# Optimization experiments

Measured on AMD Instinct MI355X. Metric: run time of the kernel, lower is better.

The kernel has to match this reference:

```python
import jax, jax.numpy as jnp
import numpy as np

N_NODES = 50000
N_EDGES = 800000
F_IN = 64
HID = 256
N_GRAPHS = 128
N_OUT = 24


def _sage_conv(x, src, dst, deg_inv, wl, bl, wr):
    # PyG SAGEConv (aggr='mean'): out = lin_l(mean_{j in N(i)} x_j) + lin_r(x_i)
    agg = jax.ops.segment_sum(x[src], dst, num_segments=x.shape[0]) * deg_inv
    return agg @ wl.T + bl + x @ wr.T


def setup_inputs() -> dict:
    key = jax.random.key(0)
    ks = jax.random.split(key, 16)
    x = jax.random.normal(ks[0], (N_NODES, F_IN), dtype=jnp.float32)
    edge_index = jax.random.randint(ks[1], (2, N_EDGES), 0, N_NODES, dtype=jnp.int64)
    batch = jnp.sort(jax.random.randint(ks[2], (N_NODES,), 0, N_GRAPHS, dtype=jnp.int64))

    def lin(k, fan_out, fan_in):
        bound = 1.0 / np.sqrt(fan_in)
        return jax.random.uniform(k, (fan_out, fan_in), jnp.float32, -bound, bound)

    inp = {
        'x': x, 'edge_index': edge_index, 'batch': batch,
        'w1l': lin(ks[3], HID, F_IN), 'b1': jnp.zeros((HID,), jnp.float32), 'w1r': lin(ks[4], HID, F_IN),
        'w2l': lin(ks[5], HID, HID), 'b2': jnp.zeros((HID,), jnp.float32), 'w2r': lin(ks[6], HID, HID),
        'w3l': lin(ks[7], HID, HID), 'b3': jnp.zeros((HID,), jnp.float32), 'w3r': lin(ks[8], HID, HID),
        'lin1_w': lin(ks[9], HID // 2, HID), 'lin1_b': jnp.zeros((HID // 2,), jnp.float32),
        'lin2_w': lin(ks[10], N_OUT, HID // 2), 'lin2_b': jnp.zeros((N_OUT,), jnp.float32),
    }
    return inp


def reference(x, edge_index, batch, w1l, b1, w1r, w2l, b2, w2r, w3l, b3, w3r,
              lin1_w, lin1_b, lin2_w, lin2_b):
    src, dst = edge_index[0], edge_index[1]
    deg = jax.ops.segment_sum(jnp.ones((src.shape[0],), jnp.float32), dst, num_segments=x.shape[0])
    deg_inv = (1.0 / jnp.maximum(deg, 1.0))[:, None]  # [N,1]

    h = jax.nn.relu(_sage_conv(x, src, dst, deg_inv, w1l, b1, w1r))
    h = jax.nn.relu(_sage_conv(h, src, dst, deg_inv, w2l, b2, w2r))
    h = jax.nn.relu(_sage_conv(h, src, dst, deg_inv, w3l, b3, w3r))

    # global mean pool over graphs
    pooled_sum = jax.ops.segment_sum(h, batch, num_segments=N_GRAPHS)
    counts = jax.ops.segment_sum(jnp.ones((h.shape[0],), jnp.float32), batch, num_segments=N_GRAPHS)
    pooled = pooled_sum / jnp.maximum(counts, 1.0)[:, None]

    g = jax.nn.relu(pooled @ lin1_w.T + lin1_b)
    return g @ lin2_w.T + lin2_b
```

## Files before the change

### kernel.cpp

```cpp
#include <hip/hip_runtime.h>

#define N_NODES 50000
#define M_PAD   50048
#define N_EDGES 800000
#define F_IN 64
#define HID 256
#define N_GRAPHS 128
#define N_OUT 24

typedef unsigned short ushort_t;
typedef __attribute__((ext_vector_type(8))) unsigned short us8;
typedef __attribute__((ext_vector_type(8))) __bf16 bf16x8;
typedef __attribute__((ext_vector_type(4))) float f32x4;

#define SLICE_US ((size_t)M_PAD * 32)

__device__ __forceinline__ unsigned short f2bf(float f) {
  unsigned u = __builtin_bit_cast(unsigned, f);
  return (unsigned short)((u + 0x7fffu + ((u >> 16) & 1u)) >> 16);
}
__device__ __forceinline__ float bf2f(unsigned short h) {
  return __builtin_bit_cast(float, (unsigned)h << 16);
}

__device__ __forceinline__ f32x4 mfma_bf16(us8 a, us8 b, f32x4 c) {
  return __builtin_amdgcn_mfma_f32_16x16x32_bf16(
      __builtin_bit_cast(bf16x8, a), __builtin_bit_cast(bf16x8, b), c, 0, 0, 0);
}

__device__ __forceinline__ void gload16(const ushort_t* g, ushort_t* l) {
  __builtin_amdgcn_global_load_lds(
      (const __attribute__((address_space(1))) void*)g,
      (__attribute__((address_space(3))) void*)l, 16, 0, 0);
}


__global__ void k_hist(const int* __restrict__ dst, int* __restrict__ deg_priv,
                       int* __restrict__ rank) {
  int e = blockIdx.x * 256 + threadIdx.x;
  if (e < N_EDGES) {
    int c = blockIdx.x & 7;
    rank[e] = atomicAdd(&deg_priv[c * N_NODES + dst[e]], 1);
  }
}

__global__ void k_gofs(const int* __restrict__ batch, int* __restrict__ gofs) {
  int t = threadIdx.x;
  if (t > N_GRAPHS) return;
  int lo = 0, hi = N_NODES;
  while (lo < hi) {
    int mid = (lo + hi) >> 1;
    if (batch[mid] < t) lo = mid + 1;
    else hi = mid;
  }
  gofs[t] = lo;
}

__global__ __launch_bounds__(1024) void k_scan1(int* __restrict__ deg_priv,
                                                int* __restrict__ deg,
                                                int* __restrict__ rowptr,
                                                int* __restrict__ partial) {
  __shared__ int s[1024];
  int t = threadIdx.x;
  int idx = blockIdx.x * 1024 + t;
  int v = 0;
  if (idx < N_NODES) {
    int run = 0;
#pragma unroll
    for (int c = 0; c < 8; ++c) {
      int dv = deg_priv[c * N_NODES + idx];
      deg_priv[c * N_NODES + idx] = run;
      run += dv;
    }
    deg[idx] = run;
    v = run;
  }
  s[t] = v;
  __syncthreads();
  for (int off = 1; off < 1024; off <<= 1) {
    int a = (t >= off) ? s[t - off] : 0;
    __syncthreads();
    s[t] += a;
    __syncthreads();
  }
  if (idx < N_NODES) rowptr[idx] = s[t] - v;
  if (t == 1023) partial[blockIdx.x] = s[1023];
}

__global__ void k_scan2(int* __restrict__ partial, int* __restrict__ rowptr) {
  __shared__ int s[64];
  int t = threadIdx.x;
  const int NB = (N_NODES + 1023) / 1024;
  int v = (t < NB) ? partial[t] : 0;
  s[t] = v;
  __syncthreads();
  for (int off = 1; off < 64; off <<= 1) {
    int a = (t >= off) ? s[t - off] : 0;
    __syncthreads();
    s[t] += a;
    __syncthreads();
  }
  if (t < NB) partial[t] = s[t] - v;
  if (t == NB - 1) rowptr[N_NODES] = s[t];
}

__global__ __launch_bounds__(1024) void k_scan3(const int* __restrict__ deg,
                                                const int* __restrict__ partial,
                                                int* __restrict__ rowptr,
                                                float* __restrict__ deg_inv) {
  int idx = blockIdx.x * 1024 + threadIdx.x;
  if (idx < N_NODES) {
    rowptr[idx] += partial[blockIdx.x];
    deg_inv[idx] = 1.0f / fmaxf((float)deg[idx], 1.0f);
  }
}

__global__ void k_place(const int* __restrict__ src, const int* __restrict__ dst,
                        const int* __restrict__ rowptr, const int* __restrict__ deg_priv,
                        const int* __restrict__ rank, int* __restrict__ esrc) {
  int e = blockIdx.x * 256 + threadIdx.x;
  if (e < N_EDGES) {
    int c = blockIdx.x & 7;
    int d = dst[e];
    esrc[rowptr[d] + deg_priv[c * N_NODES + d] + rank[e]] = src[e];
  }
}


__global__ void k_prep_x(const float* __restrict__ x, ushort_t* __restrict__ xio) {
  int g = blockIdx.x * 256 + threadIdx.x;
  if (g >= N_NODES * 8) return;
  int row = g >> 3, kb = g & 7;
  const float* p = x + (size_t)row * F_IN + kb * 8;
  us8 H, L;
#pragma unroll
  for (int i = 0; i < 8; ++i) {
    float f = p[i];
    unsigned short hi = f2bf(f);
    H[i] = hi;
    L[i] = f2bf(f - bf2f(hi));
  }
  size_t ob = (size_t)row * 128 + (size_t)((kb ^ (row & 7)) << 3);
  *(us8*)&xio[ob] = H;
  *(us8*)&xio[ob + 64] = L;
}

__global__ void k_prep_w(const float* __restrict__ w1lp, const float* __restrict__ w1rp,
                         const float* __restrict__ w2lp, const float* __restrict__ w2rp,
                         const float* __restrict__ w3lp, const float* __restrict__ w3rp,
                         ushort_t* __restrict__ wf1, ushort_t* __restrict__ wf2,
                         ushort_t* __restrict__ wf3) {
  int layer = blockIdx.z, side = blockIdx.y;
  const int Kg = (layer == 0) ? 8 : 32;
  const int qcs = Kg >> 2;
  int g = blockIdx.x * 256 + threadIdx.x;
  if (g >= 256 * Kg) return;
  const float* src = (layer == 0) ? (side ? w1rp : w1lp)
                   : (layer == 1) ? (side ? w2rp : w2lp)
                                  : (side ? w3rp : w3lp);
  ushort_t* dstf = (layer == 0) ? wf1 : (layer == 1) ? wf2 : wf3;
  int row = g / Kg, gb = g % Kg;
  const float* p = src + (size_t)row * (Kg * 8) + gb * 8;
  us8 H, L;
#pragma unroll
  for (int i = 0; i < 8; ++i) {
    float f = p[i];
    unsigned short hi = f2bf(f);
    H[i] = hi;
    L[i] = f2bf(f - bf2f(hi));
  }
  int nb2 = side * 16 + (row >> 4);
  int lane = (row & 15) + ((gb & 3) << 4);
  size_t base = ((size_t)(nb2 * qcs + (gb >> 2)) * 2) * 512 + lane * 8;
  *(us8*)&dstf[base] = H;
  *(us8*)&dstf[base + 512] = L;
}


__global__ __launch_bounds__(256) void k_agg64s(const float* __restrict__ x,
                                                const int* __restrict__ rowptr,
                                                const int* __restrict__ esrc,
                                                const float* __restrict__ deg_inv,
                                                ushort_t* __restrict__ oio) {
  int node = blockIdx.x * 4 + (threadIdx.x >> 6);
  if (node >= N_NODES) return;
  int lane = threadIdx.x & 63;
  int e0 = rowptr[node], e1 = rowptr[node + 1];
  float acc = 0.f;
  int e = e0;
  for (; e + 4 <= e1; e += 4) {
    int s0 = esrc[e], s1 = esrc[e + 1], s2 = esrc[e + 2], s3 = esrc[e + 3];
    float v0 = x[(size_t)s0 * F_IN + lane];
    float v1 = x[(size_t)s1 * F_IN + lane];
    float v2 = x[(size_t)s2 * F_IN + lane];
    float v3 = x[(size_t)s3 * F_IN + lane];
    acc += v0 + v1 + v2 + v3;
  }
  for (; e < e1; ++e) acc += x[(size_t)esrc[e] * F_IN + lane];
  acc *= deg_inv[node];
  unsigned short hi = f2bf(acc);
  unsigned short lo = f2bf(acc - bf2f(hi));
  size_t rb = (size_t)node * 128;
  int slot = ((lane >> 3) ^ (node & 7)) << 3;
  oio[rb + slot + (lane & 7)] = hi;
  oio[rb + 64 + slot + (lane & 7)] = lo;
}

__global__ __launch_bounds__(256) void k_agg256s(const ushort_t* __restrict__ hio,
                                                 const int* __restrict__ rowptr,
                                                 const int* __restrict__ esrc,
                                                 const float* __restrict__ deg_inv,
                                                 ushort_t* __restrict__ oio) {
  int c = blockIdx.x & 7;
  const ushort_t* hs = hio + (size_t)c * SLICE_US;
  ushort_t* os = oio + (size_t)c * SLICE_US;
  int q = threadIdx.x & 3;
  int ns = threadIdx.x >> 2;
  for (int base = (blockIdx.x >> 3) * 64; base < N_NODES; base += 16384) {
    int node = base + ns;
    if (node >= N_NODES) continue;
    int e0 = rowptr[node], e1 = rowptr[node + 1];
    float a[8] = {0.f, 0.f, 0.f, 0.f, 0.f, 0.f, 0.f, 0.f};
    int e = e0;
#pragma unroll 1
    for (; e + 4 <= e1; e += 4) {
      int s0 = esrc[e], s1 = esrc[e + 1], s2 = esrc[e + 2], s3 = esrc[e + 3];
      us8 v0 = *(const us8*)&hs[(size_t)s0 * 32 + ((q ^ (s0 & 3)) << 3)];
      us8 v1 = *(const us8*)&hs[(size_t)s1 * 32 + ((q ^ (s1 & 3)) << 3)];
      us8 v2 = *(const us8*)&hs[(size_t)s2 * 32 + ((q ^ (s2 & 3)) << 3)];
      us8 v3 = *(const us8*)&hs[(size_t)s3 * 32 + ((q ^ (s3 & 3)) << 3)];
#pragma unroll
      for (int i = 0; i < 8; ++i)
        a[i] += (bf2f(v0[i]) + bf2f(v1[i])) + (bf2f(v2[i]) + bf2f(v3[i]));
    }
    for (; e < e1; ++e) {
      int s = esrc[e];
      us8 v = *(const us8*)&hs[(size_t)s * 32 + ((q ^ (s & 3)) << 3)];
#pragma unroll
      for (int i = 0; i < 8; ++i) a[i] += bf2f(v[i]);
    }
    float di = deg_inv[node];
    us8 H;
#pragma unroll
    for (int i = 0; i < 8; ++i) H[i] = f2bf(a[i] * di);
    __builtin_nontemporal_store(
        H, (us8*)&os[(size_t)node * 32 + ((q ^ (node & 3)) << 3)]);
  }
}


template <int SA>
__global__ __launch_bounds__(256, 2) void k_gemm_mfma(
    const ushort_t* __restrict__ A1, int k1g, const ushort_t* __restrict__ w1f,
    const ushort_t* __restrict__ A2, int k2g, const ushort_t* __restrict__ w2f,
    const float* __restrict__ bias, ushort_t* __restrict__ oio,
    float* __restrict__ ofp, int mode) {
  __shared__ __align__(16) ushort_t ldsA[2][SA ? 16384 : 8192];

  int t = threadIdx.x;
  int wv = t >> 6, lane = t & 63;
  int fr = lane & 15, kq = lane >> 4;
  int bm = blockIdx.x;
  int rowA0 = bm * 128;

  f32x4 acc[8][4];
#pragma unroll
  for (int m = 0; m < 8; ++m)
#pragma unroll
    for (int n = 0; n < 4; ++n) acc[m][n] = (f32x4)0.f;

  const int ns1 = k1g >> 3, ns2 = k2g >> 3, ns = ns1 + ns2;
  const int lj = lane & 7, lr8 = lane >> 3;

  auto stage = [&](int buf, int s) {
    bool p2 = s >= ns1;
    const ushort_t* A = p2 ? A2 : A1;
    int Kg = p2 ? k2g : k1g;
    int sl = p2 ? (s - ns1) : s;
#pragma unroll
    for (int i = 0; i < 4; ++i) {
      int row = wv * 32 + i * 8 + lr8;
      int R = rowA0 + row;
      int lo = (wv * 32 + i * 8) * 64;
      if (SA) {
        size_t offA = ((size_t)R * (Kg * 2) + sl * 8 + lj) * 8;
        gload16(A + offA, &ldsA[buf][lo]);
        gload16(A + offA + (size_t)Kg * 8, &ldsA[buf][8192 + lo]);
      } else {
        size_t offA = (size_t)(sl * 2 + ((lj >> 2) ^ ((R >> 2) & 1))) * SLICE_US +
                      (size_t)R * 32 + (size_t)((lj & 3) << 3);
        gload16(A + offA, &ldsA[buf][lo]);
      }
    }
  };

  stage(0, 0);
  __syncthreads();
  int cur = 0;

  for (int s = 0; s < ns; ++s) {
    bool p2 = s >= ns1;
    const ushort_t* Wf = p2 ? w2f : w1f;
    int sl = p2 ? (s - ns1) : s;
    int qcs = (p2 ? k2g : k1g) >> 2;

    us8 bh[2][4], bl[2][4];
#pragma unroll
    for (int kc = 0; kc < 2; ++kc)
#pragma unroll
      for (int n = 0; n < 4; ++n) {
        size_t base = ((size_t)((wv * 4 + n) * qcs + sl * 2 + kc) * 2) * 512 + lane * 8;
        bh[kc][n] = *(const us8*)&Wf[base];
        bl[kc][n] = *(const us8*)&Wf[base + 512];
      }

    if (s + 1 < ns) stage(cur ^ 1, s + 1);

#pragma unroll
    for (int kc = 0; kc < 2; ++kc) {
      int kg = kc * 4 + kq;
      int swk = (kg ^ (fr & 7)) << 3;
#pragma unroll
      for (int mh = 0; mh < 2; ++mh) {
        us8 ah[4], al[4];
#pragma unroll
        for (int m = 0; m < 4; ++m) {
          int off = ((mh * 64 + m * 16 + fr) << 6) + swk;
          ah[m] = *(const us8*)&ldsA[cur][off];
          if (SA) al[m] = *(const us8*)&ldsA[cur][8192 + off];
        }
#pragma unroll
        for (int m = 0; m < 4; ++m)
#pragma unroll
          for (int n = 0; n < 4; ++n)
            acc[mh * 4 + m][n] = mfma_bf16(ah[m], bh[kc][n], acc[mh * 4 + m][n]);
#pragma unroll
        for (int m = 0; m < 4; ++m)
#pragma unroll
          for (int n = 0; n < 4; ++n)
            acc[mh * 4 + m][n] = mfma_bf16(ah[m], bl[kc][n], acc[mh * 4 + m][n]);
        if (SA) {
#pragma unroll
          for (int m = 0; m < 4; ++m)
#pragma unroll
            for (int n = 0; n < 4; ++n)
              acc[mh * 4 + m][n] = mfma_bf16(al[m], bh[kc][n], acc[mh * 4 + m][n]);
        }
      }
    }
    __syncthreads();
    cur ^= 1;
  }

  float bv4[4];
#pragma unroll
  for (int n = 0; n < 4; ++n) bv4[n] = bias[wv * 64 + n * 16 + fr];

  if (mode == 0) {
    ushort_t* eb = &ldsA[0][0] + wv * 2048;
#pragma unroll
    for (int c = 0; c < 4; ++c) {
      __syncthreads();
#pragma unroll
      for (int mm = 0; mm < 2; ++mm) {
#pragma unroll
        for (int n = 0; n < 4; ++n) {
          f32x4 v = acc[c * 2 + mm][n];
#pragma unroll
          for (int r = 0; r < 4; ++r)
            eb[(mm * 16 + kq * 4 + r) * 64 + n * 16 + fr] =
                f2bf(fmaxf(v[r] + bv4[n], 0.f));
        }
      }
      __syncthreads();
#pragma unroll
      for (int j = 0; j < 4; ++j) {
        int rl = j * 8 + (lane >> 3);
        int g8 = lane & 7;
        us8 v = *(const us8*)&eb[rl * 64 + g8 * 8];
        int R = bm * 128 + c * 32 + rl;
        int gi = wv * 8 + g8;
        if (R < N_NODES) {
          size_t addr = (size_t)(gi >> 2) * SLICE_US + (size_t)R * 32 +
                        (size_t)(((gi & 3) ^ (R & 3)) << 3);
          *(us8*)&oio[addr] = v;
        }
      }
    }
  } else {
    float* ebf = (float*)&ldsA[0][0] + wv * 2048;
#pragma unroll
    for (int c = 0; c < 4; ++c) {
      __syncthreads();
#pragma unroll
      for (int mm = 0; mm < 2; ++mm) {
#pragma unroll
        for (int n = 0; n < 4; ++n) {
          f32x4 v = acc[c * 2 + mm][n];
#pragma unroll
          for (int r = 0; r < 4; ++r)
            ebf[(mm * 16 + kq * 4 + r) * 64 + n * 16 + fr] =
                fmaxf(v[r] + bv4[n], 0.f);
        }
      }
      __syncthreads();
#pragma unroll
      for (int j = 0; j < 8; ++j) {
        int rl = j * 4 + (lane >> 4);
        int seg = lane & 15;
        f32x4 v = *(const f32x4*)&ebf[rl * 64 + seg * 4];
        int R = bm * 128 + c * 32 + rl;
        if (R < N_NODES)
          *(f32x4*)&ofp[(size_t)R * HID + wv * 64 + seg * 4] = v;
      }
    }
  }
}


__global__ __launch_bounds__(256) void k_pool(const float* __restrict__ h,
                                              const int* __restrict__ gofs,
                                              float* __restrict__ pooled) {
  int g = blockIdx.y, c = blockIdx.x;
  int r0 = gofs[g], r1 = gofs[g + 1];
  int rg = threadIdx.x >> 6, lane = threadIdx.x & 63;
  float ax = 0.f, ay = 0.f, az = 0.f, aw = 0.f;
  for (int r = r0 + c * 4 + rg; r < r1; r += 64) {
    float4 v = *(const float4*)&h[(size_t)r * HID + lane * 4];
    ax += v.x; ay += v.y; az += v.z; aw += v.w;
  }
  __shared__ float4 sm[4][64];
  sm[rg][lane] = make_float4(ax, ay, az, aw);
  __syncthreads();
  if (rg == 0) {
    float4 s0 = sm[0][lane], s1 = sm[1][lane], s2 = sm[2][lane], s3 = sm[3][lane];
    float* p = &pooled[g * HID + lane * 4];
    atomicAdd(p + 0, s0.x + s1.x + s2.x + s3.x);
    atomicAdd(p + 1, s0.y + s1.y + s2.y + s3.y);
    atomicAdd(p + 2, s0.z + s1.z + s2.z + s3.z);
    atomicAdd(p + 3, s0.w + s1.w + s2.w + s3.w);
  }
}


__global__ __launch_bounds__(128) void k_head(const float* __restrict__ pooled,
                                              const int* __restrict__ gofs,
                                              const float* __restrict__ w1,
                                              const float* __restrict__ b1,
                                              const float* __restrict__ w2,
                                              const float* __restrict__ b2,
                                              float* __restrict__ out) {
  __shared__ float p[HID];
  __shared__ float g1[HID / 2];
  int g = blockIdx.x, t = threadIdx.x;
  float inv = 1.f / fmaxf((float)(gofs[g + 1] - gofs[g]), 1.f);
  p[t] = pooled[g * HID + t] * inv;
  p[t + 128] = pooled[g * HID + 128 + t] * inv;
  __syncthreads();
  float s = b1[t];
#pragma unroll 4
  for (int k = 0; k < HID; ++k) s = fmaf(p[k], w1[t * HID + k], s);
  g1[t] = fmaxf(s, 0.f);
  __syncthreads();
  if (t < N_OUT) {
    float s2 = b2[t];
#pragma unroll 4
    for (int k = 0; k < HID / 2; ++k) s2 = fmaf(g1[k], w2[t * (HID / 2) + k], s2);
    out[g * N_OUT + t] = s2;
  }
}


extern "C" void kernel_launch(void* const* d_in, const int* in_sizes, int n_in,
                              void* d_out, int out_size, void* d_ws, size_t ws_size,
                              hipStream_t stream) {
  const float* x      = (const float*)d_in[0];
  const int*   ei     = (const int*)d_in[1];
  const int*   batch  = (const int*)d_in[2];
  const float* w1lw   = (const float*)d_in[3];
  const float* b1     = (const float*)d_in[4];
  const float* w1rw   = (const float*)d_in[5];
  const float* w2lw   = (const float*)d_in[6];
  const float* b2     = (const float*)d_in[7];
  const float* w2rw   = (const float*)d_in[8];
  const float* w3lw   = (const float*)d_in[9];
  const float* b3     = (const float*)d_in[10];
  const float* w3rw   = (const float*)d_in[11];
  const float* lin1_w = (const float*)d_in[12];
  const float* lin1_b = (const float*)d_in[13];
  const float* lin2_w = (const float*)d_in[14];
  const float* lin2_b = (const float*)d_in[15];
  float* out = (float*)d_out;

  const int* srcIdx = ei;
  const int* dstIdx = ei + N_EDGES;

  size_t off = 0;
  auto carve = [&](size_t bytes) {
    size_t r = off;
    off += (bytes + 255) & ~(size_t)255;
    return r;
  };
  char* ws = (char*)d_ws;
  int*      deg_priv = (int*)(ws + carve((size_t)8 * N_NODES * 4));
  int*      deg      = (int*)(ws + carve((size_t)N_NODES * 4));
  int*      rank     = (int*)(ws + carve((size_t)N_EDGES * 4));
  int*      rowptr   = (int*)(ws + carve((size_t)(N_NODES + 1) * 4));
  float*    deg_inv  = (float*)(ws + carve((size_t)N_NODES * 4));
  int*      esrc     = (int*)(ws + carve((size_t)N_EDGES * 4));
  int*      partial  = (int*)(ws + carve(64 * 4));
  int*      gofs     = (int*)(ws + carve((N_GRAPHS + 1) * 4));
  ushort_t* xio      = (ushort_t*)(ws + carve((size_t)M_PAD * 128 * 2));
  ushort_t* agg1     = (ushort_t*)(ws + carve((size_t)M_PAD * 128 * 2));
  ushort_t* agg      = (ushort_t*)(ws + carve((size_t)M_PAD * 256 * 2));
  char*     h1blk    = ws + carve((size_t)M_PAD * HID * 4);
  ushort_t* h1       = (ushort_t*)h1blk;
  float*    h3       = (float*)h1blk;
  ushort_t* h2       = (ushort_t*)(ws + carve((size_t)M_PAD * 256 * 2));
  ushort_t* wf1      = (ushort_t*)(ws + carve((size_t)2 * 32768 * 2));
  ushort_t* wf2      = (ushort_t*)(ws + carve((size_t)2 * 131072 * 2));
  ushort_t* wf3      = (ushort_t*)(ws + carve((size_t)2 * 131072 * 2));
  float*    pooled   = (float*)(ws + carve((size_t)N_GRAPHS * HID * 4));
  (void)ws_size; (void)n_in; (void)in_sizes; (void)out_size;

  hipMemsetAsync(deg_priv, 0, (size_t)8 * N_NODES * 4, stream);
  hipMemsetAsync(pooled, 0, (size_t)N_GRAPHS * HID * 4, stream);

  const int EB = (N_EDGES + 255) / 256;
  const int SB = (N_NODES + 1023) / 1024;

  k_hist<<<EB, 256, 0, stream>>>(dstIdx, deg_priv, rank);
  k_gofs<<<1, 256, 0, stream>>>(batch, gofs);
  k_scan1<<<SB, 1024, 0, stream>>>(deg_priv, deg, rowptr, partial);
  k_scan2<<<1, 64, 0, stream>>>(partial, rowptr);
  k_scan3<<<SB, 1024, 0, stream>>>(deg, partial, rowptr, deg_inv);
  k_place<<<EB, 256, 0, stream>>>(srcIdx, dstIdx, rowptr, deg_priv, rank, esrc);

  k_prep_x<<<(N_NODES * 8 + 255) / 256, 256, 0, stream>>>(x, xio);
  k_prep_w<<<dim3(32, 2, 3), 256, 0, stream>>>(w1lw, w1rw, w2lw, w2rw, w3lw, w3rw,
                                               wf1, wf2, wf3);

  const int GB = (N_NODES + 127) / 128;
  const int AB = N_NODES / 4;
  const int AGB = 2048;

  k_agg64s<<<AB, 256, 0, stream>>>(x, rowptr, esrc, deg_inv, agg1);
  k_gemm_mfma<1><<<GB, 256, 0, stream>>>(agg1, 8, wf1,
                                         xio, 8, wf1 + 32768,
                                         b1, h1, nullptr, 0);
  k_agg256s<<<AGB, 256, 0, stream>>>(h1, rowptr, esrc, deg_inv, agg);
  k_gemm_mfma<0><<<GB, 256, 0, stream>>>(agg, 32, wf2,
                                         h1, 32, wf2 + 131072,
                                         b2, h2, nullptr, 0);
  k_agg256s<<<AGB, 256, 0, stream>>>(h2, rowptr, esrc, deg_inv, agg);
  k_gemm_mfma<0><<<GB, 256, 0, stream>>>(agg, 32, wf3,
                                         h2, 32, wf3 + 131072,
                                         b3, nullptr, h3, 1);

  k_pool<<<dim3(16, N_GRAPHS), 256, 0, stream>>>(h3, gofs, pooled);
  k_head<<<N_GRAPHS, 128, 0, stream>>>(pooled, gofs, lin1_w, lin1_b, lin2_w, lin2_b, out);
}
```

Measured before the change: 314.0 us.

## Sort nodes by degree so aggregation waves process balanced workloads

Adds a counting sort of nodes by in-degree (histogram, scan, place kernels) producing a permutation. The aggregation kernels iterate over this permutation so lanes in a wave handle nodes with similar edge counts, reducing loop divergence and imbalance. It costs three extra small launches and makes output row writes scattered rather than sequential.

```diff
diff --git a/kernel.cpp b/kernel.cpp
--- a/kernel.cpp
+++ b/kernel.cpp
@@ -123,6 +123,55 @@
     int c = blockIdx.x & 7;
     int d = dst[e];
     esrc[rowptr[d] + deg_priv[c * N_NODES + d] + rank[e]] = src[e];
+  }
+}
+
+
+__global__ __launch_bounds__(1024) void k_dhist(const int* __restrict__ deg,
+                                                int* __restrict__ blockhist) {
+  __shared__ int h[64];
+  int t = threadIdx.x;
+  if (t < 64) h[t] = 0;
+  __syncthreads();
+  int idx = blockIdx.x * 1024 + t;
+  if (idx < N_NODES) atomicAdd(&h[min(deg[idx], 63)], 1);
+  __syncthreads();
+  if (t < 64) blockhist[blockIdx.x * 64 + t] = h[t];
+}
+
+__global__ void k_dscan(const int* __restrict__ blockhist, int* __restrict__ blockbase) {
+  __shared__ int tot[64];
+  __shared__ int ofs[65];
+  int t = threadIdx.x;
+  const int NB = (N_NODES + 1023) / 1024;
+  int s = 0;
+  for (int b = 0; b < NB; ++b) s += blockhist[b * 64 + t];
+  tot[t] = s;
+  __syncthreads();
+  if (t == 0) {
+    ofs[0] = 0;
+    for (int i = 0; i < 64; ++i) ofs[i + 1] = ofs[i] + tot[i];
+  }
+  __syncthreads();
+  int run = ofs[t];
+  for (int b = 0; b < NB; ++b) {
+    blockbase[b * 64 + t] = run;
+    run += blockhist[b * 64 + t];
+  }
+}
+
+__global__ __launch_bounds__(1024) void k_dplace(const int* __restrict__ deg,
+                                                 const int* __restrict__ blockbase,
+                                                 int* __restrict__ perm) {
+  __shared__ int cur[64];
+  int t = threadIdx.x;
+  if (t < 64) cur[t] = blockbase[blockIdx.x * 64 + t];
+  __syncthreads();
+  int idx = blockIdx.x * 1024 + t;
+  if (idx < N_NODES) {
+    int bin = min(deg[idx], 63);
+    int pos = atomicAdd(&cur[bin], 1);
+    perm[pos] = idx;
   }
 }
 
@@ -181,9 +230,11 @@
                                                 const int* __restrict__ rowptr,
                                                 const int* __restrict__ esrc,
                                                 const float* __restrict__ deg_inv,
+                                                const int* __restrict__ perm,
                                                 ushort_t* __restrict__ oio) {
-  int node = blockIdx.x * 4 + (threadIdx.x >> 6);
-  if (node >= N_NODES) return;
+  int slot = blockIdx.x * 4 + (threadIdx.x >> 6);
+  if (slot >= N_NODES) return;
+  int node = perm[slot];
   int lane = threadIdx.x & 63;
   int e0 = rowptr[node], e1 = rowptr[node + 1];
   float acc = 0.f;
@@ -201,15 +252,16 @@
   unsigned short hi = f2bf(acc);
   unsigned short lo = f2bf(acc - bf2f(hi));
   size_t rb = (size_t)node * 128;
-  int slot = ((lane >> 3) ^ (node & 7)) << 3;
-  oio[rb + slot + (lane & 7)] = hi;
-  oio[rb + 64 + slot + (lane & 7)] = lo;
+  int slotk = ((lane >> 3) ^ (node & 7)) << 3;
+  oio[rb + slotk + (lane & 7)] = hi;
+  oio[rb + 64 + slotk + (lane & 7)] = lo;
 }
 
 __global__ __launch_bounds__(256) void k_agg256s(const ushort_t* __restrict__ hio,
                                                  const int* __restrict__ rowptr,
                                                  const int* __restrict__ esrc,
                                                  const float* __restrict__ deg_inv,
+                                                 const int* __restrict__ perm,
                                                  ushort_t* __restrict__ oio) {
   int c = blockIdx.x & 7;
   const ushort_t* hs = hio + (size_t)c * SLICE_US;
@@ -217,8 +269,9 @@
   int q = threadIdx.x & 3;
   int ns = threadIdx.x >> 2;
   for (int base = (blockIdx.x >> 3) * 64; base < N_NODES; base += 16384) {
-    int node = base + ns;
-    if (node >= N_NODES) continue;
+    int slot = base + ns;
+    if (slot >= N_NODES) continue;
+    int node = perm[slot];
     int e0 = rowptr[node], e1 = rowptr[node + 1];
     float a[8] = {0.f, 0.f, 0.f, 0.f, 0.f, 0.f, 0.f, 0.f};
     int e = e0;
@@ -510,6 +563,9 @@
   int*      esrc     = (int*)(ws + carve((size_t)N_EDGES * 4));
   int*      partial  = (int*)(ws + carve(64 * 4));
   int*      gofs     = (int*)(ws + carve((N_GRAPHS + 1) * 4));
+  int*      blockhist= (int*)(ws + carve((size_t)49 * 64 * 4));
+  int*      blockbase= (int*)(ws + carve((size_t)49 * 64 * 4));
+  int*      perm     = (int*)(ws + carve((size_t)N_NODES * 4));
   ushort_t* xio      = (ushort_t*)(ws + carve((size_t)M_PAD * 128 * 2));
   ushort_t* agg1     = (ushort_t*)(ws + carve((size_t)M_PAD * 128 * 2));
   ushort_t* agg      = (ushort_t*)(ws + carve((size_t)M_PAD * 256 * 2));
@@ -536,6 +592,10 @@
   k_scan3<<<SB, 1024, 0, stream>>>(deg, partial, rowptr, deg_inv);
   k_place<<<EB, 256, 0, stream>>>(srcIdx, dstIdx, rowptr, deg_priv, rank, esrc);
 
+  k_dhist<<<SB, 1024, 0, stream>>>(deg, blockhist);
+  k_dscan<<<1, 64, 0, stream>>>(blockhist, blockbase);
+  k_dplace<<<SB, 1024, 0, stream>>>(deg, blockbase, perm);
+
   k_prep_x<<<(N_NODES * 8 + 255) / 256, 256, 0, stream>>>(x, xio);
   k_prep_w<<<dim3(32, 2, 3), 256, 0, stream>>>(w1lw, w1rw, w2lw, w2rw, w3lw, w3rw,
                                                wf1, wf2, wf3);
@@ -544,15 +604,15 @@
   const int AB = N_NODES / 4;
   const int AGB = 2048;
 
-  k_agg64s<<<AB, 256, 0, stream>>>(x, rowptr, esrc, deg_inv, agg1);
+  k_agg64s<<<AB, 256, 0, stream>>>(x, rowptr, esrc, deg_inv, perm, agg1);
   k_gemm_mfma<1><<<GB, 256, 0, stream>>>(agg1, 8, wf1,
                                          xio, 8, wf1 + 32768,
                                          b1, h1, nullptr, 0);
-  k_agg256s<<<AGB, 256, 0, stream>>>(h1, rowptr, esrc, deg_inv, agg);
+  k_agg256s<<<AGB, 256, 0, stream>>>(h1, rowptr, esrc, deg_inv, perm, agg);
   k_gemm_mfma<0><<<GB, 256, 0, stream>>>(agg, 32, wf2,
                                          h1, 32, wf2 + 131072,
                                          b2, h2, nullptr, 0);
-  k_agg256s<<<AGB, 256, 0, stream>>>(h2, rowptr, esrc, deg_inv, agg);
+  k_agg256s<<<AGB, 256, 0, stream>>>(h2, rowptr, esrc, deg_inv, perm, agg);
   k_gemm_mfma<0><<<GB, 256, 0, stream>>>(agg, 32, wf3,
                                          h2, 32, wf3 + 131072,
                                          b3, nullptr, h3, 1);
```

Result: slower. 344.3 us (+9.7%).
